# Performance work log

Measured on AMD Instinct MI355X. Metric: run time of the kernel, lower is better.

Reference implementation:

```python
import jax, jax.numpy as jnp
import numpy as np

NUM_LABELS = 3   # init kwarg num_labels
# init kwarg p = 1.0 -> always equalize (deterministic reference)
NUM_BINS = 256


def _equalize_channel(chan):
    """Torchvision-style histogram equalization of one uint8 channel.

    chan: int32 [H, W] with values in [0, 255].
    """
    # per-channel histogram (scatter-add into 256 bins)
    hist = jnp.zeros(NUM_BINS, jnp.int32).at[chan.ravel()].add(1)
    total = hist.sum()
    # value at the last nonzero bin: nonzero_hist[:-1].sum() == total - hist[last_nonzero]
    last_nz = (NUM_BINS - 1) - jnp.argmax((hist > 0)[::-1])
    step = (total - hist[last_nz]) // (NUM_BINS - 1)
    # LUT = floor((cumsum(hist) + step//2) / step), shifted right by one, clamped
    cum = jnp.cumsum(hist)
    lut = (cum + step // 2) // jnp.maximum(step, 1)
    lut = jnp.clip(jnp.concatenate([jnp.zeros(1, lut.dtype), lut[:-1]]), 0, NUM_BINS - 1)
    # step == 0 -> identity (torchvision early-return)
    return jnp.where(step == 0, chan, lut[chan])


def setup_inputs() -> dict:
    key = jax.random.key(0)
    # 3 RGB-like channels in [0, 255) + 3 label channels, CHW
    image = jax.random.uniform(key, (3 + NUM_LABELS, 2048, 4096), jnp.float32) * 255.0
    return {"image": image}


def reference(image):
    sample = image[:-NUM_LABELS].astype(jnp.int32)   # mimics .to(torch.uint8) truncation
    targets = image[-NUM_LABELS:]
    sample_eq = jax.vmap(_equalize_channel)(sample).astype(jnp.float32)
    return jnp.concatenate([sample_eq, targets], axis=0)
```

## Files before the change

### kernel.cpp

```cpp
#include <hip/hip_runtime.h>

#define IMG_H 2048
#define IMG_W 4096
#define CH_ELEMS (IMG_H * IMG_W)
#define NUM_CH 6
#define SAMPLE_CH 3
#define HBINS 256
#define HIST_BPC 512

__global__ __launch_bounds__(256) void eq_hist_kernel(
        const float* __restrict__ in, int* __restrict__ ghist) {
    __shared__ int lhist[4][HBINS];
    const int t = threadIdx.x;
    const int wave = t >> 6;
    for (int i = t; i < 4 * HBINS; i += 256) ((int*)lhist)[i] = 0;
    __syncthreads();

    const int ch  = blockIdx.x / HIST_BPC;
    const int blk = blockIdx.x % HIST_BPC;
    const float4* cin = (const float4*)(in + (size_t)ch * CH_ELEMS);
    const int n4 = CH_ELEMS / 4;

    for (int i = blk * 256 + t; i < n4; i += HIST_BPC * 256) {
        float4 v = cin[i];
        int bx = (int)v.x; bx = min(max(bx, 0), 255);
        int by = (int)v.y; by = min(max(by, 0), 255);
        int bz = (int)v.z; bz = min(max(bz, 0), 255);
        int bw = (int)v.w; bw = min(max(bw, 0), 255);
        atomicAdd(&lhist[wave][bx], 1);
        atomicAdd(&lhist[wave][by], 1);
        atomicAdd(&lhist[wave][bz], 1);
        atomicAdd(&lhist[wave][bw], 1);
    }
    __syncthreads();

    for (int i = t; i < HBINS; i += 256) {
        int s = lhist[0][i] + lhist[1][i] + lhist[2][i] + lhist[3][i];
        if (s) atomicAdd(&ghist[ch * HBINS + i], s);
    }
}

__global__ void eq_lut_kernel(const int* __restrict__ ghist,
                              float* __restrict__ glut) {
    if (threadIdx.x != 0) return;
    const int ch = blockIdx.x;
    const int* hist = ghist + ch * HBINS;
    float* lut = glut + ch * HBINS;

    int total = 0, last_nz = 0;
    for (int i = 0; i < HBINS; i++) {
        int h = hist[i];
        total += h;
        if (h > 0) last_nz = i;
    }
    int step = (total - hist[last_nz]) / (HBINS - 1);
    if (step == 0) {
        for (int i = 0; i < HBINS; i++) lut[i] = (float)i;
        return;
    }
    lut[0] = 0.0f;
    int cum = 0;
    const int half = step / 2;
    for (int i = 1; i < HBINS; i++) {
        cum += hist[i - 1];
        int v = (cum + half) / step;
        v = min(max(v, 0), 255);
        lut[i] = (float)v;
    }
}

__global__ __launch_bounds__(256) void eq_apply_kernel(
        const float* __restrict__ in, const float* __restrict__ glut,
        float* __restrict__ out) {
    __shared__ float slut[SAMPLE_CH * HBINS];
    for (int i = threadIdx.x; i < SAMPLE_CH * HBINS; i += 256)
        slut[i] = glut[i];
    __syncthreads();

    const float4* in4 = (const float4*)in;
    float4* out4 = (float4*)out;
    const int n4    = NUM_CH * CH_ELEMS / 4;
    const int ch_n4 = CH_ELEMS / 4;

    for (int i = blockIdx.x * 256 + threadIdx.x; i < n4; i += gridDim.x * 256) {
        float4 v = in4[i];
        const int ch = i / ch_n4;
        if (ch < SAMPLE_CH) {
            const float* l = slut + ch * HBINS;
            int bx = (int)v.x; bx = min(max(bx, 0), 255);
            int by = (int)v.y; by = min(max(by, 0), 255);
            int bz = (int)v.z; bz = min(max(bz, 0), 255);
            int bw = (int)v.w; bw = min(max(bw, 0), 255);
            v.x = l[bx]; v.y = l[by]; v.z = l[bz]; v.w = l[bw];
        }
        out4[i] = v;
    }
}

extern "C" void kernel_launch(void* const* d_in, const int* in_sizes, int n_in,
                              void* d_out, int out_size, void* d_ws, size_t ws_size,
                              hipStream_t stream) {
    const float* image = (const float*)d_in[0];
    float* out = (float*)d_out;

    int*   hist = (int*)d_ws;
    float* lut  = (float*)((char*)d_ws + SAMPLE_CH * HBINS * sizeof(int));

    hipMemsetAsync(hist, 0, SAMPLE_CH * HBINS * sizeof(int), stream);

    eq_hist_kernel<<<SAMPLE_CH * HIST_BPC, 256, 0, stream>>>(image, hist);
    eq_lut_kernel<<<SAMPLE_CH, 64, 0, stream>>>(hist, lut);
    eq_apply_kernel<<<4096, 256, 0, stream>>>(image, lut, out);
}
```

Before: 373.8 us.

## Cache quantized bytes in pass one and fuse label copy with histogram

The histogram pass now also writes a packed 8-bit copy of the sample channels and copies the label channels straight to the output. The apply pass then reads those compact bytes instead of re-reading the float image. Global histogram atomics and the memset are replaced by per-block partial histograms, which a parallel scan-based LUT kernel reduces. This cuts HBM traffic and serial LUT work, at the cost of a workspace buffer and extra partial-histogram storage.

```diff
diff --git a/kernel.cpp b/kernel.cpp
--- a/kernel.cpp
+++ b/kernel.cpp
@@ -3,97 +3,122 @@
 #define IMG_H 2048
 #define IMG_W 4096
 #define CH_ELEMS (IMG_H * IMG_W)
+#define CH_N4    (CH_ELEMS / 4)
 #define NUM_CH 6
 #define SAMPLE_CH 3
 #define HBINS 256
-#define HIST_BPC 512
+#define BPC 512
 
-__global__ __launch_bounds__(256) void eq_hist_kernel(
-        const float* __restrict__ in, int* __restrict__ ghist) {
-    __shared__ int lhist[4][HBINS];
-    const int t = threadIdx.x;
+#define WS_LUT_OFF  (2u << 20)
+#define WS_U8_OFF   (4u << 20)
+
+__global__ __launch_bounds__(256) void eq_pass1_kernel(
+        const float* __restrict__ in, float* __restrict__ out,
+        unsigned* __restrict__ u8buf, int* __restrict__ parts) {
+    const int t   = threadIdx.x;
+    const int ch  = blockIdx.x / BPC;
+    const int blk = blockIdx.x % BPC;
+
+    if (ch >= SAMPLE_CH) {
+        const float4* src = (const float4*)(in + (size_t)ch * CH_ELEMS);
+        float4*       dst = (float4*)(out + (size_t)ch * CH_ELEMS);
+        for (int i = blk * 256 + t; i < CH_N4; i += BPC * 256)
+            dst[i] = src[i];
+        return;
+    }
+
+    __shared__ int lh[4][HBINS];
     const int wave = t >> 6;
-    for (int i = t; i < 4 * HBINS; i += 256) ((int*)lhist)[i] = 0;
+    for (int i = t; i < 4 * HBINS; i += 256) ((int*)lh)[i] = 0;
     __syncthreads();
 
-    const int ch  = blockIdx.x / HIST_BPC;
-    const int blk = blockIdx.x % HIST_BPC;
-    const float4* cin = (const float4*)(in + (size_t)ch * CH_ELEMS);
-    const int n4 = CH_ELEMS / 4;
+    const float4* src = (const float4*)(in + (size_t)ch * CH_ELEMS);
+    unsigned*     dst = u8buf + ch * CH_N4;
 
-    for (int i = blk * 256 + t; i < n4; i += HIST_BPC * 256) {
-        float4 v = cin[i];
-        int bx = (int)v.x; bx = min(max(bx, 0), 255);
-        int by = (int)v.y; by = min(max(by, 0), 255);
-        int bz = (int)v.z; bz = min(max(bz, 0), 255);
-        int bw = (int)v.w; bw = min(max(bw, 0), 255);
-        atomicAdd(&lhist[wave][bx], 1);
-        atomicAdd(&lhist[wave][by], 1);
-        atomicAdd(&lhist[wave][bz], 1);
-        atomicAdd(&lhist[wave][bw], 1);
+    for (int i = blk * 256 + t; i < CH_N4; i += BPC * 256) {
+        float4 v = src[i];
+        int b0 = (int)v.x; b0 = min(max(b0, 0), 255);
+        int b1 = (int)v.y; b1 = min(max(b1, 0), 255);
+        int b2 = (int)v.z; b2 = min(max(b2, 0), 255);
+        int b3 = (int)v.w; b3 = min(max(b3, 0), 255);
+        atomicAdd(&lh[wave][b0], 1);
+        atomicAdd(&lh[wave][b1], 1);
+        atomicAdd(&lh[wave][b2], 1);
+        atomicAdd(&lh[wave][b3], 1);
+        dst[i] = (unsigned)b0 | ((unsigned)b1 << 8) |
+                 ((unsigned)b2 << 16) | ((unsigned)b3 << 24);
     }
     __syncthreads();
 
-    for (int i = t; i < HBINS; i += 256) {
-        int s = lhist[0][i] + lhist[1][i] + lhist[2][i] + lhist[3][i];
-        if (s) atomicAdd(&ghist[ch * HBINS + i], s);
-    }
+    parts[((size_t)ch * BPC + blk) * HBINS + t] =
+        lh[0][t] + lh[1][t] + lh[2][t] + lh[3][t];
 }
 
-__global__ void eq_lut_kernel(const int* __restrict__ ghist,
-                              float* __restrict__ glut) {
-    if (threadIdx.x != 0) return;
+__global__ __launch_bounds__(256) void eq_lut_kernel(
+        const int* __restrict__ parts, float* __restrict__ glut) {
     const int ch = blockIdx.x;
-    const int* hist = ghist + ch * HBINS;
-    float* lut = glut + ch * HBINS;
+    const int t  = threadIdx.x;
+    const int* p = parts + (size_t)ch * BPC * HBINS;
 
-    int total = 0, last_nz = 0;
-    for (int i = 0; i < HBINS; i++) {
-        int h = hist[i];
-        total += h;
-        if (h > 0) last_nz = i;
+    int h = 0;
+    #pragma unroll 8
+    for (int j = 0; j < BPC; j++) h += p[j * HBINS + t];
+
+    __shared__ int sh[HBINS];
+    __shared__ int sc[HBINS];
+    __shared__ int nz[HBINS];
+    sh[t] = h;
+    sc[t] = h;
+    nz[t] = (h > 0) ? t : 0;
+    __syncthreads();
+
+    for (int off = 1; off < HBINS; off <<= 1) {
+        int add = (t >= off) ? sc[t - off] : 0;
+        __syncthreads();
+        sc[t] += add;
+        __syncthreads();
     }
-    int step = (total - hist[last_nz]) / (HBINS - 1);
+    for (int off = HBINS / 2; off >= 1; off >>= 1) {
+        if (t < off) nz[t] = max(nz[t], nz[t + off]);
+        __syncthreads();
+    }
+
+    const int total   = sc[HBINS - 1];
+    const int last_nz = nz[0];
+    const int step    = (total - sh[last_nz]) / (HBINS - 1);
+
+    float outv;
     if (step == 0) {
-        for (int i = 0; i < HBINS; i++) lut[i] = (float)i;
-        return;
+        outv = (float)t;
+    } else if (t == 0) {
+        outv = 0.0f;
+    } else {
+        int v = (sc[t - 1] + (step >> 1)) / step;
+        outv = (float)min(v, 255);
     }
-    lut[0] = 0.0f;
-    int cum = 0;
-    const int half = step / 2;
-    for (int i = 1; i < HBINS; i++) {
-        cum += hist[i - 1];
-        int v = (cum + half) / step;
-        v = min(max(v, 0), 255);
-        lut[i] = (float)v;
-    }
+    glut[ch * HBINS + t] = outv;
 }
 
 __global__ __launch_bounds__(256) void eq_apply_kernel(
-        const float* __restrict__ in, const float* __restrict__ glut,
+        const unsigned* __restrict__ u8buf, const float* __restrict__ glut,
         float* __restrict__ out) {
-    __shared__ float slut[SAMPLE_CH * HBINS];
+    __shared__ float sl[SAMPLE_CH * HBINS];
     for (int i = threadIdx.x; i < SAMPLE_CH * HBINS; i += 256)
-        slut[i] = glut[i];
+        sl[i] = glut[i];
     __syncthreads();
 
-    const float4* in4 = (const float4*)in;
     float4* out4 = (float4*)out;
-    const int n4    = NUM_CH * CH_ELEMS / 4;
-    const int ch_n4 = CH_ELEMS / 4;
+    const int n = SAMPLE_CH * CH_N4;
 
-    for (int i = blockIdx.x * 256 + threadIdx.x; i < n4; i += gridDim.x * 256) {
-        float4 v = in4[i];
-        const int ch = i / ch_n4;
-        if (ch < SAMPLE_CH) {
-            const float* l = slut + ch * HBINS;
-            int bx = (int)v.x; bx = min(max(bx, 0), 255);
-            int by = (int)v.y; by = min(max(by, 0), 255);
-            int bz = (int)v.z; bz = min(max(bz, 0), 255);
-            int bw = (int)v.w; bw = min(max(bw, 0), 255);
-            v.x = l[bx]; v.y = l[by]; v.z = l[bz]; v.w = l[bw];
-        }
-        out4[i] = v;
+    for (int i = blockIdx.x * 256 + threadIdx.x; i < n; i += gridDim.x * 256) {
+        unsigned w = u8buf[i];
+        const float* l = sl + (i >> 21) * HBINS;
+        float4 o;
+        o.x = l[w & 255u];
+        o.y = l[(w >> 8) & 255u];
+        o.z = l[(w >> 16) & 255u];
+        o.w = l[w >> 24];
+        out4[i] = o;
     }
 }
 
@@ -103,12 +128,11 @@
     const float* image = (const float*)d_in[0];
     float* out = (float*)d_out;
 
-    int*   hist = (int*)d_ws;
-    float* lut  = (float*)((char*)d_ws + SAMPLE_CH * HBINS * sizeof(int));
+    int*      parts = (int*)d_ws;
+    float*    lut   = (float*)((char*)d_ws + WS_LUT_OFF);
+    unsigned* u8buf = (unsigned*)((char*)d_ws + WS_U8_OFF);
 
-    hipMemsetAsync(hist, 0, SAMPLE_CH * HBINS * sizeof(int), stream);
-
-    eq_hist_kernel<<<SAMPLE_CH * HIST_BPC, 256, 0, stream>>>(image, hist);
-    eq_lut_kernel<<<SAMPLE_CH, 64, 0, stream>>>(hist, lut);
-    eq_apply_kernel<<<4096, 256, 0, stream>>>(image, lut, out);
+    eq_pass1_kernel<<<NUM_CH * BPC, 256, 0, stream>>>(image, out, u8buf, parts);
+    eq_lut_kernel<<<SAMPLE_CH, 256, 0, stream>>>(parts, lut);
+    eq_apply_kernel<<<2048, 256, 0, stream>>>(u8buf, lut, out);
 }
```

Result: no change. 368.7 us (-1.4%).
